# Kernel tuning notes

Hardware: AMD Instinct MI355X
Metric: run time of the kernel (lower is better)

The kernel has to match this reference:

```python
import jax, jax.numpy as jnp
import numpy as np

B, T, D = 16, 1024, 256   # batch, tokens, embedding_dim
Q, K = 4, 4096            # num_quantizers, n_embed
BETA = 1.0


def l2norm(x, eps=1e-12):
    n = jnp.linalg.norm(x, axis=-1, keepdims=True)
    return x / jnp.maximum(n, eps)


def vq_stage(z, codebook):
    """NormEMAVectorQuantizer forward (eval math; EMA buffer update omitted).
    z: (B,T,D) float; codebook: (K,D) l2-normalized rows.
    Returns straight-through quantized (B,T,D), scalar commit loss, indices (N,).
    """
    zn = l2norm(z)                                   # normalize input features
    zf = zn.reshape(-1, zn.shape[-1])                # (N, D)
    # squared euclidean distances (N, K): |z|^2 + |e|^2 - 2 z.e
    d = (jnp.sum(zf * zf, axis=1, keepdims=True)
         + jnp.sum(codebook * codebook, axis=1)[None, :]
         - 2.0 * zf @ codebook.T)
    idx = jnp.argmin(d, axis=1)                      # (N,)
    z_q = codebook[idx].reshape(zn.shape)            # gather codewords
    loss = BETA * jnp.mean((jax.lax.stop_gradient(z_q) - zn) ** 2)
    z_q = zn + jax.lax.stop_gradient(z_q - zn)       # straight-through
    return z_q, loss, idx


def setup_inputs() -> dict:
    key = jax.random.key(0)
    kx, kc = jax.random.split(key)
    x = jax.random.normal(kx, (B, T, D), dtype=jnp.float32)
    # EMA codebooks are kept l2-normalized in NormEMAVectorQuantizer
    codebooks = l2norm(jax.random.normal(kc, (Q, K, D), dtype=jnp.float32))
    return {"x": x, "codebooks": codebooks}


def reference(x, codebooks):
    residual = x
    quantized_outputs, losses, indices = [], [], []
    for q in range(codebooks.shape[0]):              # fixed small stage count
        z_q, loss, idx = vq_stage(residual, codebooks[q])
        # faithful to source: value of residual is unchanged, gradient path added
        residual = residual - jax.lax.stop_gradient(z_q) + z_q
        quantized_outputs.append(z_q)
        losses.append(loss)
        indices.append(idx)
    quantized_sum = quantized_outputs[0]
    for t in quantized_outputs[1:]:
        quantized_sum = quantized_sum + t
    total_loss = losses[0]
    for l in losses[1:]:
        total_loss = total_loss + l
    return quantized_sum, total_loss, jnp.stack(indices, axis=1)  # (N, Q) int
```

## Files before the change

kernel.cpp:

```cpp
#include <hip/hip_runtime.h>
#include <stdint.h>


#define NR 16384
#define DIM 256
#define KCB 4096
#define QST 4
#define MARGIN_DOT 4e-4f
#define MARGIN2_DOT 2e-5f
#define CAPL 4096

typedef _Float16 f16;
typedef __attribute__((ext_vector_type(4))) f16 f16x4;
typedef __attribute__((ext_vector_type(8))) f16 f16x8;
typedef __attribute__((ext_vector_type(4))) float f32x4;

#define WS_ZN_HI   ((size_t)0)
#define WS_ZN_LO   ((size_t)8*1024*1024)
#define WS_CB_HI   ((size_t)16*1024*1024)
#define WS_CB_LO   ((size_t)24*1024*1024)
#define WS_NORMS   ((size_t)32*1024*1024)
#define WS_SSQ     (WS_NORMS + 65536)
#define WS_TOPS    (WS_SSQ + 65536)
#define WS_IDX     (WS_TOPS + (size_t)QST*NR*2*16)
#define WS_LIST    (WS_IDX + (size_t)QST*NR*4)
#define WS_LIST2   (WS_LIST + (size_t)QST*CAPL*4)
#define WS_TOPS2   (WS_LIST2 + (size_t)QST*NR*4)
#define WS_CNT     (WS_TOPS2 + (size_t)QST*CAPL*8*16)
#define WS_PART    (WS_CNT + 64)
#define WS_TOPS3   (WS_PART + 16384)

__device__ __forceinline__ void gll16(const void* g, void* l) {
  __builtin_amdgcn_global_load_lds(
      (const __attribute__((address_space(1))) void*)g,
      (__attribute__((address_space(3))) void*)l, 16, 0, 0);
}

__device__ __forceinline__ float dot4chain(const float4* __restrict__ c,
                                           const float4* __restrict__ z) {
  float dot = 0.f;
  for (int d = 0; d < 64; ++d) {
    const float4 cv = c[d], zv = z[d];
    dot += cv.x * zv.x + cv.y * zv.y + cv.z * zv.z + cv.w * zv.w;
  }
  return dot;
}

__global__ void prep_kernel(const float* __restrict__ x, const float* __restrict__ cb,
                            char* __restrict__ ws) {
  const int w = threadIdx.x >> 6, lane = threadIdx.x & 63;
  const int normalize = (blockIdx.x < (NR / 4));
  const int blk = normalize ? blockIdx.x : blockIdx.x - (NR / 4);
  const float* src = normalize ? x : cb;
  const int row = blk * 4 + w;
  const float4 v = ((const float4*)src)[row * 64 + lane];
  float ss = v.x * v.x + v.y * v.y + v.z * v.z + v.w * v.w;
#pragma unroll
  for (int m = 32; m; m >>= 1) ss += __shfl_xor(ss, m);
  float4 z = v;
  f16 *hi, *lo;
  if (normalize) {
    const float denom = fmaxf(sqrtf(ss), 1e-12f);
    z.x = v.x / denom; z.y = v.y / denom; z.z = v.z / denom; z.w = v.w / denom;
    hi = (f16*)(ws + WS_ZN_HI); lo = (f16*)(ws + WS_ZN_LO);
    if (lane == 0) ((float*)(ws + WS_NORMS))[row] = denom;
    if (blockIdx.x == 0 && threadIdx.x < 8) ((int*)(ws + WS_CNT))[threadIdx.x] = 0;
  } else {
    hi = (f16*)(ws + WS_CB_HI); lo = (f16*)(ws + WS_CB_LO);
    if (lane == 0) ((float*)(ws + WS_SSQ))[row] = ss;
  }
  f16x4 h, l;
  h[0] = (f16)z.x; h[1] = (f16)z.y; h[2] = (f16)z.z; h[3] = (f16)z.w;
  l[0] = (f16)(z.x - (float)h[0]); l[1] = (f16)(z.y - (float)h[1]);
  l[2] = (f16)(z.z - (float)h[2]); l[3] = (f16)(z.w - (float)h[3]);
  ((f16x4*)hi)[row * 64 + lane] = h;
  ((f16x4*)lo)[row * 64 + lane] = l;
}

__launch_bounds__(256, 2)
__global__ void score_kernel(char* __restrict__ ws) {
  __shared__ __align__(16) f16 smem[2][128][64];
  const int tid = threadIdx.x, w = tid >> 6, lane = tid & 63;
  const int wr = w >> 1, wc = w & 1;
  const int blk = blockIdx.x;
  const int xcd = blk & 7, st = xcd >> 1;
  const int rowtile = ((xcd & 1) << 6) + (blk >> 3);
  const int rowBase = rowtile << 7;

  const f16* zn_hi = (const f16*)(ws + WS_ZN_HI);
  const f16* cb_hi = (const f16*)(ws + WS_CB_HI);

  const int reg = w >> 1;
  const int half = w & 1;
  const f16* src = reg ? cb_hi : zn_hi;
  const int g0 = (lane & 7) ^ ((lane >> 3) & 7);
  const size_t laneOff = (size_t)(lane >> 3) * DIM + (size_t)g0 * 8;
  f16* ldsW = &smem[reg][half * 64][0];

  float t1[16], t2[16]; int i1[16];
#pragma unroll
  for (int s = 0; s < 16; ++s) { t1[s] = -3.4e38f; t2[s] = -3.4e38f; i1[s] = 0; }
  const int colLane = wc * 64 + (lane & 15);

  for (int ct = 0; ct < 32; ++ct) {
    f32x4 acc[4][4];
#pragma unroll
    for (int m = 0; m < 4; ++m)
#pragma unroll
      for (int n = 0; n < 4; ++n) { acc[m][n][0] = 0.f; acc[m][n][1] = 0.f; acc[m][n][2] = 0.f; acc[m][n][3] = 0.f; }

    const int rowG0 = (reg ? (st * KCB + ct * 128) : rowBase) + half * 64;
    const f16* srcBase = src + (size_t)rowG0 * DIM + laneOff;

    for (int dc = 0; dc < 4; ++dc) {
      __syncthreads();
      const f16* sp = srcBase + dc * 64;
#pragma unroll
      for (int op = 0; op < 8; ++op)
        gll16(sp + op * 8 * DIM, ldsW + op * 512);
      __syncthreads();

#pragma unroll
      for (int kk = 0; kk < 2; ++kk) {
        f16x8 ah[4];
#pragma unroll
        for (int m = 0; m < 4; ++m) {
          const int rl = wr * 64 + m * 16 + (lane & 15);
          const int slot = ((kk << 2) + (lane >> 4)) ^ (rl & 7);
          ah[m] = *(const f16x8*)(&smem[0][0][0] + rl * 64 + slot * 8);
        }
#pragma unroll
        for (int n = 0; n < 4; ++n) {
          const int cl = wc * 64 + n * 16 + (lane & 15);
          const int slot = ((kk << 2) + (lane >> 4)) ^ (cl & 7);
          const f16x8 bh = *(const f16x8*)(&smem[1][0][0] + cl * 64 + slot * 8);
#pragma unroll
          for (int m = 0; m < 4; ++m)
            acc[m][n] = __builtin_amdgcn_mfma_f32_16x16x32_f16(ah[m], bh, acc[m][n], 0, 0, 0);
        }
      }
    }
#pragma unroll
    for (int n = 0; n < 4; ++n) {
      const int col = ct * 128 + n * 16 + colLane;
#pragma unroll
      for (int m = 0; m < 4; ++m)
#pragma unroll
        for (int r = 0; r < 4; ++r) {
          const float sc = acc[m][n][r];
          const int sl = m * 4 + r;
          if (sc > t1[sl]) { t2[sl] = t1[sl]; t1[sl] = sc; i1[sl] = col; }
          else t2[sl] = fmaxf(t2[sl], sc);
        }
    }
  }

  float4* tops = (float4*)(ws + WS_TOPS);
#pragma unroll
  for (int m = 0; m < 4; ++m)
#pragma unroll
    for (int r = 0; r < 4; ++r) {
      const int sl = m * 4 + r;
      float a1 = t1[sl], a2 = t2[sl]; int ai = i1[sl];
#pragma unroll
      for (int msk = 1; msk < 16; msk <<= 1) {
        const float o1 = __shfl_xor(a1, msk);
        const float o2 = __shfl_xor(a2, msk);
        const int   oi = __shfl_xor(ai, msk);
        if (o1 > a1)       { a2 = fmaxf(a1, o2); a1 = o1; ai = oi; }
        else if (o1 == a1) { a2 = a1; ai = min(ai, oi); }
        else               { a2 = fmaxf(a2, o1); }
      }
      if ((lane & 15) == 0) {
        const int row = rowBase + wr * 64 + m * 16 + (lane >> 4) * 4 + r;
        tops[((size_t)st * NR + row) * 2 + wc] =
            make_float4(a1, a2, __int_as_float(ai), 0.f);
      }
    }
}

__global__ void merge_flag_kernel(char* __restrict__ ws) {
  const int t = blockIdx.x * 256 + threadIdx.x;
  const int row = t >> 2, st = t & 3;
  const float4* tops = (const float4*)(ws + WS_TOPS);
  const float4 a = tops[((size_t)st * NR + row) * 2 + 0];
  const float4 b = tops[((size_t)st * NR + row) * 2 + 1];
  float v1, v2; int i1;
  if (a.x > b.x)      { v1 = a.x; v2 = fmaxf(a.y, b.x); i1 = __float_as_int(a.z); }
  else if (b.x > a.x) { v1 = b.x; v2 = fmaxf(b.y, a.x); i1 = __float_as_int(b.z); }
  else { v1 = a.x; v2 = a.x; i1 = min(__float_as_int(a.z), __float_as_int(b.z)); }
  ((int*)(ws + WS_IDX))[t] = i1;
  if (v1 - v2 < MARGIN_DOT) {
    const int p = atomicAdd((int*)(ws + WS_CNT) + st, 1);
    if (p < CAPL) ((int*)(ws + WS_LIST))[st * CAPL + p] = row;
    else {
      const int p2 = atomicAdd((int*)(ws + WS_CNT) + 4 + st, 1);
      ((int*)(ws + WS_LIST2))[(size_t)st * NR + p2] = row;
    }
  }
}

__launch_bounds__(256, 2)
__global__ void rescue_mfma_kernel(char* __restrict__ ws) {
  __shared__ __align__(16) f16 smem[4][128][64];
  __shared__ float mv1[2][128], mv2[2][128];
  __shared__ int   mi1[2][128];
  const int tid = threadIdx.x, w = tid >> 6, lane = tid & 63;
  const int wr = w >> 1, wc = w & 1;
  const int st = blockIdx.x & 3;
  const int kc = (blockIdx.x >> 2) & 7;
  const int slot = blockIdx.x >> 5;
  const int cnt = min(((const int*)(ws + WS_CNT))[st], CAPL);
  const int ntile = (cnt + 127) >> 7;
  const int* list = (const int*)(ws + WS_LIST) + st * CAPL;

  const f16* zn_hi = (const f16*)(ws + WS_ZN_HI);
  const f16* zn_lo = (const f16*)(ws + WS_ZN_LO);
  const f16* cb_hi = (const f16*)(ws + WS_CB_HI);
  const f16* cb_lo = (const f16*)(ws + WS_CB_LO);

  const int g0 = (lane & 7) ^ ((lane >> 3) & 7);
  const size_t laneOff = (size_t)(lane >> 3) * DIM + (size_t)g0 * 8;
  f16* ldsW = &smem[w][0][0];
  const f16* srcA = (w == 1) ? zn_lo : zn_hi;
  const f16* srcB = (w == 3) ? cb_lo : cb_hi;
  const int colLane = wc * 64 + (lane & 15);

  for (int tile = slot; tile < ntile; tile += 32) {
    const int base = tile << 7;
    int lid[16];
    if (w < 2) {
#pragma unroll
      for (int op = 0; op < 16; ++op) {
        const int i = base + op * 8 + (lane >> 3);
        lid[op] = list[min(i, cnt - 1)];
      }
    }
    float t1[16], t2[16]; int i1[16];
#pragma unroll
    for (int s = 0; s < 16; ++s) { t1[s] = -3.4e38f; t2[s] = -3.4e38f; i1[s] = 0; }

    for (int ct = kc * 4; ct < kc * 4 + 4; ++ct) {
      f32x4 acc[4][4];
#pragma unroll
      for (int m = 0; m < 4; ++m)
#pragma unroll
        for (int n = 0; n < 4; ++n) { acc[m][n][0] = 0.f; acc[m][n][1] = 0.f; acc[m][n][2] = 0.f; acc[m][n][3] = 0.f; }

      const f16* srcBBase = srcB + ((size_t)st * KCB + (size_t)ct * 128) * DIM + laneOff;

      for (int dc = 0; dc < 4; ++dc) {
        __syncthreads();
        if (w < 2) {
#pragma unroll
          for (int op = 0; op < 16; ++op)
            gll16(srcA + (size_t)lid[op] * DIM + dc * 64 + (size_t)g0 * 8,
                  ldsW + op * 512);
        } else {
          const f16* sp = srcBBase + dc * 64;
#pragma unroll
          for (int op = 0; op < 16; ++op)
            gll16(sp + op * 8 * DIM, ldsW + op * 512);
        }
        __syncthreads();

#pragma unroll
        for (int kk = 0; kk < 2; ++kk) {
          f16x8 ah[4], al[4];
#pragma unroll
          for (int m = 0; m < 4; ++m) {
            const int rl = wr * 64 + m * 16 + (lane & 15);
            const int slt = ((kk << 2) + (lane >> 4)) ^ (rl & 7);
            const int off = rl * 64 + slt * 8;
            ah[m] = *(const f16x8*)(&smem[0][0][0] + off);
            al[m] = *(const f16x8*)(&smem[1][0][0] + off);
          }
#pragma unroll
          for (int n = 0; n < 4; ++n) {
            const int cl = wc * 64 + n * 16 + (lane & 15);
            const int slt = ((kk << 2) + (lane >> 4)) ^ (cl & 7);
            const int off = cl * 64 + slt * 8;
            const f16x8 bh = *(const f16x8*)(&smem[2][0][0] + off);
            const f16x8 bl = *(const f16x8*)(&smem[3][0][0] + off);
#pragma unroll
            for (int m = 0; m < 4; ++m) {
              acc[m][n] = __builtin_amdgcn_mfma_f32_16x16x32_f16(ah[m], bh, acc[m][n], 0, 0, 0);
              acc[m][n] = __builtin_amdgcn_mfma_f32_16x16x32_f16(ah[m], bl, acc[m][n], 0, 0, 0);
              acc[m][n] = __builtin_amdgcn_mfma_f32_16x16x32_f16(al[m], bh, acc[m][n], 0, 0, 0);
            }
          }
        }
      }
#pragma unroll
      for (int n = 0; n < 4; ++n) {
        const int col = ct * 128 + n * 16 + colLane;
#pragma unroll
        for (int m = 0; m < 4; ++m)
#pragma unroll
          for (int r = 0; r < 4; ++r) {
            const float sc = acc[m][n][r];
            const int sl = m * 4 + r;
            if (sc > t1[sl]) { t2[sl] = t1[sl]; t1[sl] = sc; i1[sl] = col; }
            else t2[sl] = fmaxf(t2[sl], sc);
          }
      }
    }

#pragma unroll
    for (int m = 0; m < 4; ++m)
#pragma unroll
      for (int r = 0; r < 4; ++r) {
        const int sl = m * 4 + r;
        float a1 = t1[sl], a2 = t2[sl]; int ai = i1[sl];
#pragma unroll
        for (int msk = 1; msk < 16; msk <<= 1) {
          const float o1 = __shfl_xor(a1, msk);
          const float o2 = __shfl_xor(a2, msk);
          const int   oi = __shfl_xor(ai, msk);
          if (o1 > a1)       { a2 = fmaxf(a1, o2); a1 = o1; ai = oi; }
          else if (o1 == a1) { a2 = a1; ai = min(ai, oi); }
          else               { a2 = fmaxf(a2, o1); }
        }
        if ((lane & 15) == 0) {
          const int rloc = wr * 64 + m * 16 + (lane >> 4) * 4 + r;
          mv1[wc][rloc] = a1; mv2[wc][rloc] = a2; mi1[wc][rloc] = ai;
        }
      }
    __syncthreads();
    if (tid < 128 && base + tid < cnt) {
      const float a1 = mv1[0][tid], a2 = mv2[0][tid]; const int ai = mi1[0][tid];
      const float b1 = mv1[1][tid], b2 = mv2[1][tid]; const int bi = mi1[1][tid];
      float v1, v2; int fi;
      if (a1 > b1)      { v1 = a1; v2 = fmaxf(a2, b1); fi = ai; }
      else if (b1 > a1) { v1 = b1; v2 = fmaxf(b2, a1); fi = bi; }
      else { v1 = a1; v2 = a1; fi = min(ai, bi); }
      ((float4*)(ws + WS_TOPS2))[((size_t)(st * CAPL + base + tid) << 3) + kc] =
          make_float4(v1, v2, __int_as_float(fi), 0.f);
    }
    __syncthreads();
  }
}

__global__ void rescue_merge_kernel(char* __restrict__ ws) {
  const int t = blockIdx.x * 256 + threadIdx.x;
  const int st = t >> 12, j = t & (CAPL - 1);
  const int cnt = min(((const int*)(ws + WS_CNT))[st], CAPL);
  if (j >= cnt) return;
  const float4* p = (const float4*)(ws + WS_TOPS2) + ((size_t)(st * CAPL + j) << 3);
  float V1 = -3.4e38f, V2 = -3.4e38f; int I1 = 0;
#pragma unroll
  for (int c = 0; c < 8; ++c) {
    const float4 e = p[c];
    const float v1 = e.x, v2 = e.y; const int i1 = __float_as_int(e.z);
    if (v1 > V1) { V2 = fmaxf(V1, v2); V1 = v1; I1 = i1; }
    else {
      if (v1 == V1) I1 = min(I1, i1);
      V2 = fmaxf(V2, v1);
    }
  }
  const int row = ((const int*)(ws + WS_LIST))[st * CAPL + j];
  ((int*)(ws + WS_IDX))[row * 4 + st] = I1;
  if (V1 - V2 < MARGIN2_DOT) {
    const int p2 = atomicAdd((int*)(ws + WS_CNT) + 4 + st, 1);
    ((int*)(ws + WS_LIST2))[(size_t)st * NR + p2] = row;
  }
}

__global__ void rescue_exact_kernel(const float* __restrict__ x, const float* __restrict__ cb,
                                    char* __restrict__ ws) {
  __shared__ __align__(16) float zrow[DIM];
  __shared__ float zsq_s;
  __shared__ float lbv[4];
  __shared__ int   lbi[4];
  const int tid = threadIdx.x, w = tid >> 6, lane = tid & 63;
  const int st = blockIdx.x & 3;
  const int kc = (blockIdx.x >> 2) & 15;
  const int slot = blockIdx.x >> 6;
  const int cnt = min(((const int*)(ws + WS_CNT))[4 + st], CAPL);
  const int* list = (const int*)(ws + WS_LIST2) + (size_t)st * NR;
  const float* cbs = cb + (size_t)st * KCB * DIM;
  const float* ssqp = (const float*)(ws + WS_SSQ) + (size_t)st * KCB;
  int2* part = (int2*)(ws + WS_TOPS3);

  for (int j = slot; j < cnt; j += 16) {
    const int row = list[j];
    if (tid < 32) {
      const float denom = ((const float*)(ws + WS_NORMS))[row];
      const int g = tid;
      float ss = 0.f;
#pragma unroll
      for (int e = 0; e < 8; ++e) {
        const float v = x[(size_t)row * DIM + g * 8 + e] / denom;
        zrow[g * 8 + e] = v;
        ss += v * v;
      }
#pragma unroll
      for (int m = 16; m; m >>= 1) ss += __shfl_xor(ss, m);
      if (g == 0) zsq_s = ss;
    }
    __syncthreads();
    const float zsq = zsq_s;
    const int k = kc * 256 + tid;
    const float dot = dot4chain((const float4*)(cbs + (size_t)k * DIM), (const float4*)zrow);
    float bd = (zsq + ssqp[k]) - 2.0f * dot;
    int bi = k;
#pragma unroll
    for (int m = 32; m; m >>= 1) {
      const float od = __shfl_xor(bd, m);
      const int   oi = __shfl_xor(bi, m);
      if (od < bd || (od == bd && oi < bi)) { bd = od; bi = oi; }
    }
    if (lane == 0) { lbv[w] = bd; lbi[w] = bi; }
    __syncthreads();
    if (tid == 0) {
      float fb = lbv[0]; int fi = lbi[0];
#pragma unroll
      for (int ww = 1; ww < 4; ++ww)
        if (lbv[ww] < fb || (lbv[ww] == fb && lbi[ww] < fi)) { fb = lbv[ww]; fi = lbi[ww]; }
      part[((size_t)(st * CAPL + j) << 4) + kc] = make_int2(__float_as_int(fb), fi);
    }
    __syncthreads();
  }
}

__global__ void rescue_exact_merge_kernel(char* __restrict__ ws) {
  const int t = blockIdx.x * 256 + threadIdx.x;
  const int st = t >> 12, j = t & (CAPL - 1);
  const int cnt = min(((const int*)(ws + WS_CNT))[4 + st], CAPL);
  if (j >= cnt) return;
  const int2* part = (const int2*)(ws + WS_TOPS3) + ((size_t)(st * CAPL + j) << 4);
  float fb = 3.4e38f; int fi = 0x7fffffff;
#pragma unroll
  for (int kc = 0; kc < 16; ++kc) {
    const int2 e = part[kc];
    const float d = __int_as_float(e.x);
    if (d < fb || (d == fb && e.y < fi)) { fb = d; fi = e.y; }
  }
  const int row = ((const int*)(ws + WS_LIST2))[(size_t)st * NR + j];
  ((int*)(ws + WS_IDX))[row * 4 + st] = fi;
}

__global__ void rescue_tail_kernel(const float* __restrict__ x, const float* __restrict__ cb,
                                   char* __restrict__ ws) {
  __shared__ __align__(16) float zrows[8][DIM];
  __shared__ float zsqs[8];
  __shared__ float lbv[4][8];
  __shared__ int   lbi[4][8];
  const int tid = threadIdx.x, w = tid >> 6, lane = tid & 63;
  const int st = blockIdx.x & 3, slot = blockIdx.x >> 2;
  const int cnt = ((const int*)(ws + WS_CNT))[4 + st] - CAPL;
  if (cnt <= 0) return;
  const int nch = (cnt + 7) >> 3;
  const int* list = (const int*)(ws + WS_LIST2) + (size_t)st * NR + CAPL;
  const float* cbs = cb + (size_t)st * KCB * DIM;
  const float* ssqp = (const float*)(ws + WS_SSQ) + (size_t)st * KCB;

  for (int ch = slot; ch < nch; ch += 16) {
    const int base = ch * 8;
    const int nr = min(8, cnt - base);
    const int r = tid >> 5, g = tid & 31;
    if (r < nr) {
      const int row = list[base + r];
      const float denom = ((const float*)(ws + WS_NORMS))[row];
      float ss = 0.f;
#pragma unroll
      for (int j = 0; j < 8; ++j) {
        const float v = x[(size_t)row * DIM + g * 8 + j] / denom;
        zrows[r][g * 8 + j] = v;
        ss += v * v;
      }
#pragma unroll
      for (int m = 16; m; m >>= 1) ss += __shfl_xor(ss, m);
      if (g == 0) zsqs[r] = ss;
    }
    __syncthreads();

    float bd[8]; int bix[8];
#pragma unroll
    for (int q = 0; q < 8; ++q) { bd[q] = 3.4e38f; bix[q] = 0x7fffffff; }

    for (int k = tid; k < KCB; k += 256) {
      const float4* cr = (const float4*)(cbs + (size_t)k * DIM);
      const float4* zr = (const float4*)&zrows[0][0];
      float dot[8];
#pragma unroll
      for (int q = 0; q < 8; ++q) dot[q] = 0.f;
      for (int d = 0; d < 64; ++d) {
        const float4 cv = cr[d];
#pragma unroll
        for (int q = 0; q < 8; ++q) {
          const float4 zv = zr[q * 64 + d];
          dot[q] += cv.x * zv.x + cv.y * zv.y + cv.z * zv.z + cv.w * zv.w;
        }
      }
      const float sk = ssqp[k];
#pragma unroll
      for (int q = 0; q < 8; ++q) {
        const float dist = (zsqs[q] + sk) - 2.0f * dot[q];
        if (dist < bd[q]) { bd[q] = dist; bix[q] = k; }
      }
    }
#pragma unroll
    for (int q = 0; q < 8; ++q) {
#pragma unroll
      for (int m = 32; m; m >>= 1) {
        const float od = __shfl_xor(bd[q], m);
        const int   oi = __shfl_xor(bix[q], m);
        if (od < bd[q] || (od == bd[q] && oi < bix[q])) { bd[q] = od; bix[q] = oi; }
      }
      if (lane == 0) { lbv[w][q] = bd[q]; lbi[w][q] = bix[q]; }
    }
    __syncthreads();
    if (tid < 8 && tid < nr) {
      float fb = lbv[0][tid]; int fi = lbi[0][tid];
#pragma unroll
      for (int ww = 1; ww < 4; ++ww) {
        const float od = lbv[ww][tid]; const int oi = lbi[ww][tid];
        if (od < fb || (od == fb && oi < fi)) { fb = od; fi = oi; }
      }
      const int row = list[base + tid];
      ((int*)(ws + WS_IDX))[row * 4 + st] = fi;
    }
    __syncthreads();
  }
}

__global__ void finalize_kernel(const float* __restrict__ x, const float* __restrict__ cb,
                                char* __restrict__ ws, float* __restrict__ out) {
  __shared__ float wsum[4];
  const int w = threadIdx.x >> 6, lane = threadIdx.x & 63;
  const int row = blockIdx.x * 4 + w;
  const int* idxp = (const int*)(ws + WS_IDX) + (size_t)row * 4;
  const float denom = ((const float*)(ws + WS_NORMS))[row];
  const float4 xv = ((const float4*)x)[row * 64 + lane];
  const float4 zn = make_float4(xv.x / denom, xv.y / denom, xv.z / denom, xv.w / denom);
  float4 s = make_float4(0.f, 0.f, 0.f, 0.f);
  float lacc = 0.f;
#pragma unroll
  for (int q = 0; q < 4; ++q) {
    const int id = idxp[q];
    const float4 e = ((const float4*)(cb + ((size_t)q * KCB + id) * DIM))[lane];
    s.x += e.x; s.y += e.y; s.z += e.z; s.w += e.w;
    const float dx = e.x - zn.x, dy = e.y - zn.y, dz = e.z - zn.z, dw = e.w - zn.w;
    lacc += dx * dx + dy * dy + dz * dz + dw * dw;
  }
  ((float4*)out)[row * 64 + lane] = s;
  if (lane < 4) out[4194305 + (size_t)row * 4 + lane] = (float)idxp[lane];
#pragma unroll
  for (int m = 32; m; m >>= 1) lacc += __shfl_xor(lacc, m);
  if (lane == 0) wsum[w] = lacc;
  __syncthreads();
  if (threadIdx.x == 0)
    ((float*)(ws + WS_PART))[blockIdx.x] = wsum[0] + wsum[1] + wsum[2] + wsum[3];
}

__global__ void loss_final_kernel(const char* __restrict__ ws, float* __restrict__ out) {
  __shared__ float wsum[4];
  const int tid = threadIdx.x, w = tid >> 6, lane = tid & 63;
  const float* p = (const float*)(ws + WS_PART);
  float s = 0.f;
  for (int i = tid; i < 4096; i += 256) s += p[i];
#pragma unroll
  for (int m = 32; m; m >>= 1) s += __shfl_xor(s, m);
  if (lane == 0) wsum[w] = s;
  __syncthreads();
  if (tid == 0)
    out[4194304] = (wsum[0] + wsum[1] + wsum[2] + wsum[3]) * (1.0f / 4194304.0f);
}

extern "C" void kernel_launch(void* const* d_in, const int* in_sizes, int n_in,
                              void* d_out, int out_size, void* d_ws, size_t ws_size,
                              hipStream_t stream) {
  (void)in_sizes; (void)n_in; (void)out_size; (void)ws_size;
  const float* x = (const float*)d_in[0];
  const float* cb = (const float*)d_in[1];
  float* out = (float*)d_out;
  char* ws = (char*)d_ws;

  hipLaunchKernelGGL(prep_kernel, dim3(NR / 2), dim3(256), 0, stream, x, cb, ws);
  hipLaunchKernelGGL(score_kernel, dim3(512), dim3(256), 0, stream, ws);
  hipLaunchKernelGGL(merge_flag_kernel, dim3((NR * QST) / 256), dim3(256), 0, stream, ws);
  hipLaunchKernelGGL(rescue_mfma_kernel, dim3(1024), dim3(256), 0, stream, ws);
  hipLaunchKernelGGL(rescue_merge_kernel, dim3((QST * CAPL) / 256), dim3(256), 0, stream, ws);
  hipLaunchKernelGGL(rescue_exact_kernel, dim3(1024), dim3(256), 0, stream, x, cb, ws);
  hipLaunchKernelGGL(rescue_exact_merge_kernel, dim3((QST * CAPL) / 256), dim3(256), 0, stream, ws);
  hipLaunchKernelGGL(rescue_tail_kernel, dim3(64), dim3(256), 0, stream, x, cb, ws);
  hipLaunchKernelGGL(finalize_kernel, dim3(NR / 4), dim3(256), 0, stream, x, cb, ws, out);
  hipLaunchKernelGGL(loss_final_kernel, dim3(1), dim3(256), 0, stream, ws, out);
}
```

Before: 372.6 us.

## Double-buffer score kernel LDS loads and fuse top-2 merge into epilogue

The score kernel now double-buffers its shared-memory tiles. It issues the global-to-LDS load for the next K-chunk before computing on the current one, which removes one barrier per chunk and lets loads overlap MFMA work. The separate merge_flag kernel is folded into the score kernel's epilogue: the two column-half top-2 results are merged through LDS, and the kernel writes the indices and rescue lists directly. This saves a launch and the round-trip through the tops buffer. The cost is double the LDS footprint (64KB per block), which may limit occupancy at launch_bounds(256,2).

```diff
diff --git a/kernel.cpp b/kernel.cpp
--- a/kernel.cpp
+++ b/kernel.cpp
@@ -79,7 +79,7 @@
 
 __launch_bounds__(256, 2)
 __global__ void score_kernel(char* __restrict__ ws) {
-  __shared__ __align__(16) f16 smem[2][128][64];
+  __shared__ __align__(16) f16 smem[2][2][128][64];
   const int tid = threadIdx.x, w = tid >> 6, lane = tid & 63;
   const int wr = w >> 1, wc = w & 1;
   const int blk = blockIdx.x;
@@ -92,75 +92,90 @@
 
   const int reg = w >> 1;
   const int half = w & 1;
-  const f16* src = reg ? cb_hi : zn_hi;
   const int g0 = (lane & 7) ^ ((lane >> 3) & 7);
   const size_t laneOff = (size_t)(lane >> 3) * DIM + (size_t)g0 * 8;
-  f16* ldsW = &smem[reg][half * 64][0];
+  const f16* srcA0 = zn_hi + (size_t)(rowBase + half * 64) * DIM + laneOff;
+  const f16* srcB0 = cb_hi + ((size_t)st * KCB + half * 64) * DIM + laneOff;
 
   float t1[16], t2[16]; int i1[16];
 #pragma unroll
   for (int s = 0; s < 16; ++s) { t1[s] = -3.4e38f; t2[s] = -3.4e38f; i1[s] = 0; }
   const int colLane = wc * 64 + (lane & 15);
 
-  for (int ct = 0; ct < 32; ++ct) {
-    f32x4 acc[4][4];
-#pragma unroll
-    for (int m = 0; m < 4; ++m)
-#pragma unroll
-      for (int n = 0; n < 4; ++n) { acc[m][n][0] = 0.f; acc[m][n][1] = 0.f; acc[m][n][2] = 0.f; acc[m][n][3] = 0.f; }
-
-    const int rowG0 = (reg ? (st * KCB + ct * 128) : rowBase) + half * 64;
-    const f16* srcBase = src + (size_t)rowG0 * DIM + laneOff;
-
-    for (int dc = 0; dc < 4; ++dc) {
-      __syncthreads();
-      const f16* sp = srcBase + dc * 64;
-#pragma unroll
-      for (int op = 0; op < 8; ++op)
-        gll16(sp + op * 8 * DIM, ldsW + op * 512);
-      __syncthreads();
-
-#pragma unroll
-      for (int kk = 0; kk < 2; ++kk) {
-        f16x8 ah[4];
-#pragma unroll
-        for (int m = 0; m < 4; ++m) {
-          const int rl = wr * 64 + m * 16 + (lane & 15);
-          const int slot = ((kk << 2) + (lane >> 4)) ^ (rl & 7);
-          ah[m] = *(const f16x8*)(&smem[0][0][0] + rl * 64 + slot * 8);
-        }
-#pragma unroll
-        for (int n = 0; n < 4; ++n) {
-          const int cl = wc * 64 + n * 16 + (lane & 15);
-          const int slot = ((kk << 2) + (lane >> 4)) ^ (cl & 7);
-          const f16x8 bh = *(const f16x8*)(&smem[1][0][0] + cl * 64 + slot * 8);
+  auto STAGE = [&](int b, int r) {
+    const int ct = r >> 2, dc = r & 3;
+    const f16* sp = reg ? (srcB0 + (size_t)ct * 128 * DIM + dc * 64)
+                        : (srcA0 + dc * 64);
+    f16* dst = &smem[b][reg][half * 64][0];
+#pragma unroll
+    for (int op = 0; op < 8; ++op)
+      gll16(sp + op * 8 * DIM, dst + op * 512);
+  };
+
+  STAGE(0, 0);
+  __syncthreads();
+
+  f32x4 acc[4][4];
+  const f32x4 zero4 = {0.f, 0.f, 0.f, 0.f};
+
+  for (int r = 0; r < 128; ++r) {
+    const int buf = r & 1;
+    if (r + 1 < 128) STAGE(buf ^ 1, r + 1);
+    const int dc = r & 3;
+    const f16* As = &smem[buf][0][0][0];
+    const f16* Bs = &smem[buf][1][0][0];
+#pragma unroll
+    for (int kk = 0; kk < 2; ++kk) {
+      f16x8 ah[4];
+#pragma unroll
+      for (int m = 0; m < 4; ++m) {
+        const int rl = wr * 64 + m * 16 + (lane & 15);
+        const int slot = ((kk << 2) + (lane >> 4)) ^ (rl & 7);
+        ah[m] = *(const f16x8*)(As + rl * 64 + slot * 8);
+      }
+#pragma unroll
+      for (int n = 0; n < 4; ++n) {
+        const int cl = wc * 64 + n * 16 + (lane & 15);
+        const int slot = ((kk << 2) + (lane >> 4)) ^ (cl & 7);
+        const f16x8 bh = *(const f16x8*)(Bs + cl * 64 + slot * 8);
+        if (dc == 0 && kk == 0) {
+#pragma unroll
+          for (int m = 0; m < 4; ++m)
+            acc[m][n] = __builtin_amdgcn_mfma_f32_16x16x32_f16(ah[m], bh, zero4, 0, 0, 0);
+        } else {
 #pragma unroll
           for (int m = 0; m < 4; ++m)
             acc[m][n] = __builtin_amdgcn_mfma_f32_16x16x32_f16(ah[m], bh, acc[m][n], 0, 0, 0);
         }
       }
     }
-#pragma unroll
-    for (int n = 0; n < 4; ++n) {
-      const int col = ct * 128 + n * 16 + colLane;
-#pragma unroll
-      for (int m = 0; m < 4; ++m)
-#pragma unroll
-        for (int r = 0; r < 4; ++r) {
-          const float sc = acc[m][n][r];
-          const int sl = m * 4 + r;
-          if (sc > t1[sl]) { t2[sl] = t1[sl]; t1[sl] = sc; i1[sl] = col; }
-          else t2[sl] = fmaxf(t2[sl], sc);
-        }
-    }
-  }
-
-  float4* tops = (float4*)(ws + WS_TOPS);
+    if (dc == 3) {
+      const int ct = r >> 2;
+#pragma unroll
+      for (int n = 0; n < 4; ++n) {
+        const int col = ct * 128 + n * 16 + colLane;
+#pragma unroll
+        for (int m = 0; m < 4; ++m)
+#pragma unroll
+          for (int rr = 0; rr < 4; ++rr) {
+            const float sc = acc[m][n][rr];
+            const int sl = m * 4 + rr;
+            if (sc > t1[sl]) { t2[sl] = t1[sl]; t1[sl] = sc; i1[sl] = col; }
+            else t2[sl] = fmaxf(t2[sl], sc);
+          }
+      }
+    }
+    __syncthreads();
+  }
+
+  float* mv1 = (float*)&smem[0][0][0][0];
+  float* mv2 = mv1 + 256;
+  int*   mi1v = (int*)(mv2 + 256);
 #pragma unroll
   for (int m = 0; m < 4; ++m)
 #pragma unroll
-    for (int r = 0; r < 4; ++r) {
-      const int sl = m * 4 + r;
+    for (int rr = 0; rr < 4; ++rr) {
+      const int sl = m * 4 + rr;
       float a1 = t1[sl], a2 = t2[sl]; int ai = i1[sl];
 #pragma unroll
       for (int msk = 1; msk < 16; msk <<= 1) {
@@ -172,30 +187,27 @@
         else               { a2 = fmaxf(a2, o1); }
       }
       if ((lane & 15) == 0) {
-        const int row = rowBase + wr * 64 + m * 16 + (lane >> 4) * 4 + r;
-        tops[((size_t)st * NR + row) * 2 + wc] =
-            make_float4(a1, a2, __int_as_float(ai), 0.f);
-      }
-    }
-}
-
-__global__ void merge_flag_kernel(char* __restrict__ ws) {
-  const int t = blockIdx.x * 256 + threadIdx.x;
-  const int row = t >> 2, st = t & 3;
-  const float4* tops = (const float4*)(ws + WS_TOPS);
-  const float4 a = tops[((size_t)st * NR + row) * 2 + 0];
-  const float4 b = tops[((size_t)st * NR + row) * 2 + 1];
-  float v1, v2; int i1;
-  if (a.x > b.x)      { v1 = a.x; v2 = fmaxf(a.y, b.x); i1 = __float_as_int(a.z); }
-  else if (b.x > a.x) { v1 = b.x; v2 = fmaxf(b.y, a.x); i1 = __float_as_int(b.z); }
-  else { v1 = a.x; v2 = a.x; i1 = min(__float_as_int(a.z), __float_as_int(b.z)); }
-  ((int*)(ws + WS_IDX))[t] = i1;
-  if (v1 - v2 < MARGIN_DOT) {
-    const int p = atomicAdd((int*)(ws + WS_CNT) + st, 1);
-    if (p < CAPL) ((int*)(ws + WS_LIST))[st * CAPL + p] = row;
-    else {
-      const int p2 = atomicAdd((int*)(ws + WS_CNT) + 4 + st, 1);
-      ((int*)(ws + WS_LIST2))[(size_t)st * NR + p2] = row;
+        const int rloc = wr * 64 + m * 16 + (lane >> 4) * 4 + rr;
+        mv1[wc * 128 + rloc] = a1; mv2[wc * 128 + rloc] = a2; mi1v[wc * 128 + rloc] = ai;
+      }
+    }
+  __syncthreads();
+  if (tid < 128) {
+    const float a1 = mv1[tid], a2 = mv2[tid]; const int ai = mi1v[tid];
+    const float b1 = mv1[128 + tid], b2 = mv2[128 + tid]; const int bi = mi1v[128 + tid];
+    float v1, v2; int fi;
+    if (a1 > b1)      { v1 = a1; v2 = fmaxf(a2, b1); fi = ai; }
+    else if (b1 > a1) { v1 = b1; v2 = fmaxf(b2, a1); fi = bi; }
+    else { v1 = a1; v2 = a1; fi = min(ai, bi); }
+    const int row = rowBase + tid;
+    ((int*)(ws + WS_IDX))[row * 4 + st] = fi;
+    if (v1 - v2 < MARGIN_DOT) {
+      const int p = atomicAdd((int*)(ws + WS_CNT) + st, 1);
+      if (p < CAPL) ((int*)(ws + WS_LIST))[st * CAPL + p] = row;
+      else {
+        const int p2 = atomicAdd((int*)(ws + WS_CNT) + 4 + st, 1);
+        ((int*)(ws + WS_LIST2))[(size_t)st * NR + p2] = row;
+      }
     }
   }
 }
@@ -579,7 +591,6 @@
 
   hipLaunchKernelGGL(prep_kernel, dim3(NR / 2), dim3(256), 0, stream, x, cb, ws);
   hipLaunchKernelGGL(score_kernel, dim3(512), dim3(256), 0, stream, ws);
-  hipLaunchKernelGGL(merge_flag_kernel, dim3((NR * QST) / 256), dim3(256), 0, stream, ws);
   hipLaunchKernelGGL(rescue_mfma_kernel, dim3(1024), dim3(256), 0, stream, ws);
   hipLaunchKernelGGL(rescue_merge_kernel, dim3((QST * CAPL) / 256), dim3(256), 0, stream, ws);
   hipLaunchKernelGGL(rescue_exact_kernel, dim3(1024), dim3(256), 0, stream, x, cb, ws);
```

After: 363.9 us. 1.02x faster.
